# Performance work log

Hardware: AMD Instinct MI355X
Metric: run time of the kernel (lower is better)

Reference implementation:

```python
import math
import jax, jax.numpy as jnp
import numpy as np

N_HEADS = 32
N_KV_HEADS = 8
HEAD_DIM = 128
DIM = 4096
B = 32
MAX_SEQ = 4096
Q_LEN = 1
START_POS = 4095


def setup_inputs() -> dict:
    key = jax.random.key(0)
    ks = jax.random.split(key, 9)
    x = jax.random.normal(ks[0], (B, Q_LEN, DIM), dtype=jnp.float32)
    # RoPE angles for the current positions (seqlen=Q_LEN, half head_dim pairs)
    inv_freq = 1.0 / (500000.0 ** (np.arange(0, HEAD_DIM, 2, dtype=np.float32) / HEAD_DIM))
    pos = np.arange(START_POS, START_POS + Q_LEN, dtype=np.float32)
    ang = pos[:, None] * inv_freq[None, :]  # [Q_LEN, HEAD_DIM//2]
    freqs_cos = jnp.asarray(np.cos(ang), dtype=jnp.float32)
    freqs_sin = jnp.asarray(np.sin(ang), dtype=jnp.float32)
    cache_k = jax.random.normal(ks[1], (B, MAX_SEQ, N_KV_HEADS, HEAD_DIM), dtype=jnp.float32)
    cache_v = jax.random.normal(ks[2], (B, MAX_SEQ, N_KV_HEADS, HEAD_DIM), dtype=jnp.float32)
    s = 0.02
    wq = jax.random.normal(ks[3], (N_HEADS * HEAD_DIM, DIM), dtype=jnp.float32) * s
    wk = jax.random.normal(ks[4], (N_KV_HEADS * HEAD_DIM, DIM), dtype=jnp.float32) * s
    wv = jax.random.normal(ks[5], (N_KV_HEADS * HEAD_DIM, DIM), dtype=jnp.float32) * s
    wo = jax.random.normal(ks[6], (DIM, N_HEADS * HEAD_DIM), dtype=jnp.float32) * s
    return {"x": x, "start_pos": START_POS, "freqs_cos": freqs_cos, "freqs_sin": freqs_sin,
            "cache_k": cache_k, "cache_v": cache_v, "wq": wq, "wk": wk, "wv": wv, "wo": wo}


def _rope(t, cos, sin):
    # t: [B, S, h, hd]; cos/sin: [S, hd//2]; complex multiply on (even, odd) pairs
    tr = t.reshape(*t.shape[:-1], HEAD_DIM // 2, 2)
    a, b = tr[..., 0], tr[..., 1]
    c = cos[None, :, None, :]
    s = sin[None, :, None, :]
    out = jnp.stack([a * c - b * s, a * s + b * c], axis=-1)
    return out.reshape(t.shape)


def reference(x, start_pos, freqs_cos, freqs_sin, cache_k, cache_v, wq, wk, wv, wo):
    bsz, seqlen, _ = x.shape
    n_rep = N_HEADS // N_KV_HEADS
    xq = jnp.einsum('bsd,od->bso', x, wq).reshape(bsz, seqlen, N_HEADS, HEAD_DIM)
    xk = jnp.einsum('bsd,od->bso', x, wk).reshape(bsz, seqlen, N_KV_HEADS, HEAD_DIM)
    xv = jnp.einsum('bsd,od->bso', x, wv).reshape(bsz, seqlen, N_KV_HEADS, HEAD_DIM)
    xq = _rope(xq, freqs_cos, freqs_sin)
    xk = _rope(xk, freqs_cos, freqs_sin)
    # KV-cache update (start_pos is a static Python int)
    cache_k = cache_k.at[:, start_pos:start_pos + seqlen].set(xk)
    cache_v = cache_v.at[:, start_pos:start_pos + seqlen].set(xv)
    keys = cache_k[:, :start_pos + seqlen]    # [B, T, Hkv, hd]
    values = cache_v[:, :start_pos + seqlen]  # [B, T, Hkv, hd]
    # GQA: group query heads [H] -> [Hkv, n_rep]; avoids materializing repeated KV
    q = xq.reshape(bsz, seqlen, N_KV_HEADS, n_rep, HEAD_DIM)
    scale = 1.0 / math.sqrt(HEAD_DIM)
    scores = jnp.einsum('bsgrd,btgd->bgrst', q, keys) * scale  # [B, Hkv, n_rep, S, T]
    probs = jax.nn.softmax(scores, axis=-1)
    out = jnp.einsum('bgrst,btgd->bsgrd', probs, values)
    out = out.reshape(bsz, seqlen, N_HEADS * HEAD_DIM)
    return jnp.einsum('bse,de->bsd', out, wo)
```

## Files before the change

kernel.cpp:

```cpp
#include <hip/hip_runtime.h>

#define B_    32
#define DIM_  4096
#define NH_   32
#define NKV_  8
#define HD_   128
#define TSEQ  4096
#define NQKV  6144
#define GSPLIT 16
#define BK    32
#define NT    256
#define KRANGE (DIM_ / GSPLIT)
#define KTILES (KRANGE / BK)
#define TSPL  16
#define TS    256

typedef float f4_t __attribute__((ext_vector_type(4)));

__device__ __forceinline__ f4_t ntl(const float* p) {
    return __builtin_nontemporal_load((const f4_t*)p);
}

__global__ __launch_bounds__(256) void gemm32(
    const float* __restrict__ A, const float* __restrict__ w0,
    const float* __restrict__ w1, const float* __restrict__ w2,
    int b1, int b2, int N, float* __restrict__ po)
{
    __shared__ __align__(16) float wt[BK][NT + 4];
    __shared__ __align__(16) float xp[128][33];
    const int tid = threadIdx.x;
    const int cg  = tid & 63;
    const int bg  = tid >> 6;
    const int ct  = blockIdx.x * NT;
    const int k0  = blockIdx.y * KRANGE;

    const float* wb_; int c0_;
    if (ct < b1)      { wb_ = w0; c0_ = ct; }
    else if (ct < b2) { wb_ = w1; c0_ = ct - b1; }
    else              { wb_ = w2; c0_ = ct - b2; }

    const int kqx = (tid & 31) * 4;
    const int rrx = tid >> 5;
    const int kq2 = (tid & 7) * 4;
    const int rr2 = tid >> 3;

    f4_t xreg[4], wreg[8];

    #pragma unroll
    for (int st = 0; st < 4; ++st)
        xreg[st] = *(const f4_t*)(A + (size_t)(st * 8 + rrx) * DIM_ + k0 + kqx);
    #pragma unroll
    for (int st = 0; st < 8; ++st)
        wreg[st] = ntl(wb_ + (size_t)(c0_ + st * 32 + rr2) * DIM_ + k0 + kq2);
    #pragma unroll
    for (int st = 0; st < 4; ++st) {
        const int bb = st * 8 + rrx;
        xp[kqx + 0][bb] = xreg[st][0]; xp[kqx + 1][bb] = xreg[st][1];
        xp[kqx + 2][bb] = xreg[st][2]; xp[kqx + 3][bb] = xreg[st][3];
    }
    #pragma unroll
    for (int st = 0; st < 8; ++st) {
        const int c = st * 32 + rr2;
        wt[kq2 + 0][c] = wreg[st][0]; wt[kq2 + 1][c] = wreg[st][1];
        wt[kq2 + 2][c] = wreg[st][2]; wt[kq2 + 3][c] = wreg[st][3];
    }
    __syncthreads();

    float acc[8][4];
    #pragma unroll
    for (int i = 0; i < 8; ++i)
        #pragma unroll
        for (int j = 0; j < 4; ++j) acc[i][j] = 0.f;

    for (int tt = 0; tt < KTILES; ++tt) {
        if (tt < KTILES - 1) {
            #pragma unroll
            for (int st = 0; st < 8; ++st)
                wreg[st] = ntl(wb_ + (size_t)(c0_ + st * 32 + rr2) * DIM_
                               + k0 + (tt + 1) * BK + kq2);
        }
        if (tt == 3) {
            #pragma unroll
            for (int st = 0; st < 4; ++st)
                xreg[st] = *(const f4_t*)(A + (size_t)(st * 8 + rrx) * DIM_
                                          + k0 + 128 + kqx);
        }
        #pragma unroll 8
        for (int kk = 0; kk < BK; ++kk) {
            const int kr = (tt & 3) * BK + kk;
            const float4 xa = *(const float4*)&xp[kr][bg * 8];
            const float4 xb = *(const float4*)&xp[kr][bg * 8 + 4];
            const float4 wa = *(const float4*)&wt[kk][cg * 4];
            const float xv[8] = {xa.x, xa.y, xa.z, xa.w, xb.x, xb.y, xb.z, xb.w};
            const float wv[4] = {wa.x, wa.y, wa.z, wa.w};
            #pragma unroll
            for (int i = 0; i < 8; ++i)
                #pragma unroll
                for (int j = 0; j < 4; ++j)
                    acc[i][j] = fmaf(xv[i], wv[j], acc[i][j]);
        }
        __syncthreads();
        if (tt == 3) {
            #pragma unroll
            for (int st = 0; st < 4; ++st) {
                const int bb = st * 8 + rrx;
                xp[kqx + 0][bb] = xreg[st][0]; xp[kqx + 1][bb] = xreg[st][1];
                xp[kqx + 2][bb] = xreg[st][2]; xp[kqx + 3][bb] = xreg[st][3];
            }
        }
        if (tt < KTILES - 1) {
            #pragma unroll
            for (int st = 0; st < 8; ++st) {
                const int c = st * 32 + rr2;
                wt[kq2 + 0][c] = wreg[st][0]; wt[kq2 + 1][c] = wreg[st][1];
                wt[kq2 + 2][c] = wreg[st][2]; wt[kq2 + 3][c] = wreg[st][3];
            }
            __syncthreads();
        }
    }

    const size_t srow = (size_t)blockIdx.y * B_;
    #pragma unroll
    for (int i = 0; i < 8; ++i) {
        const int b = bg * 8 + i;
        const float4 o = make_float4(acc[i][0], acc[i][1], acc[i][2], acc[i][3]);
        *(float4*)&po[(srow + b) * N + ct + cg * 4] = o;
    }
}

__global__ void reduce_rope(const float* __restrict__ po,
                            const float* __restrict__ fc, const float* __restrict__ fs,
                            float* __restrict__ qkv)
{
    const int pid = blockIdx.x * 256 + threadIdx.x;
    const int b  = pid / (NQKV / 4);
    const int c0 = (pid - b * (NQKV / 4)) * 4;
    f4_t v = {0.f, 0.f, 0.f, 0.f};
    #pragma unroll
    for (int s = 0; s < GSPLIT; ++s)
        v += *(const f4_t*)(po + ((size_t)s * B_ + b) * NQKV + c0);
    if (c0 < DIM_ + NKV_ * HD_) {
        const int i = (c0 & 127) >> 1;
        const float ca = fc[i],     sa = fs[i];
        const float cb = fc[i + 1], sb = fs[i + 1];
        f4_t o;
        o[0] = v[0] * ca - v[1] * sa;
        o[1] = v[0] * sa + v[1] * ca;
        o[2] = v[2] * cb - v[3] * sb;
        o[3] = v[2] * sb + v[3] * cb;
        v = o;
    }
    *(f4_t*)(qkv + (size_t)b * NQKV + c0) = v;
}

__device__ __forceinline__ void attn_step(const f4_t kc, const f4_t vc,
                                          const f4_t* q, f4_t* acc, float* l)
{
    float p0 = kc[0]*q[0][0] + kc[1]*q[0][1] + kc[2]*q[0][2] + kc[3]*q[0][3];
    float p1 = kc[0]*q[1][0] + kc[1]*q[1][1] + kc[2]*q[1][2] + kc[3]*q[1][3];
    float p2 = kc[0]*q[2][0] + kc[1]*q[2][1] + kc[2]*q[2][2] + kc[3]*q[2][3];
    float p3 = kc[0]*q[3][0] + kc[1]*q[3][1] + kc[2]*q[3][2] + kc[3]*q[3][3];
    #pragma unroll
    for (int off = 1; off < 32; off <<= 1) {
        p0 += __shfl_xor(p0, off);
        p1 += __shfl_xor(p1, off);
        p2 += __shfl_xor(p2, off);
        p3 += __shfl_xor(p3, off);
    }
    const float scale = 0.08838834764831845f;
    p0 = __expf(p0 * scale); p1 = __expf(p1 * scale);
    p2 = __expf(p2 * scale); p3 = __expf(p3 * scale);
    l[0] += p0; l[1] += p1; l[2] += p2; l[3] += p3;
    acc[0] += p0 * vc; acc[1] += p1 * vc;
    acc[2] += p2 * vc; acc[3] += p3 * vc;
}

__global__ __launch_bounds__(256) void attn_partial(
    const float* __restrict__ qkv, const float* __restrict__ ck,
    const float* __restrict__ cv,
    float* __restrict__ po , float* __restrict__ pl )
{
    const int blk = blockIdx.x;
    const int s = blk & (TSPL - 1);
    const int b = blk / TSPL;
    const int tid  = threadIdx.x;
    const int g    = tid >> 5;
    const int lane = tid & 31;
    const int d4   = lane * 4;
    const float* qb = qkv + (size_t)b * NQKV;

    f4_t q[4];
    #pragma unroll
    for (int h = 0; h < 4; ++h)
        q[h] = *(const f4_t*)(qb + (g * 4 + h) * HD_ + d4);

    f4_t zero4 = {0.f, 0.f, 0.f, 0.f};
    f4_t acc[4] = {zero4, zero4, zero4, zero4};
    float l[4] = {0.f, 0.f, 0.f, 0.f};

    const int t0 = s * TS;
    const bool last = (s == TSPL - 1);
    const int niter = TS - (last ? 1 : 0);

    const size_t base = ((size_t)b * TSEQ + t0) * (NKV_ * HD_) + tid * 4;
    const float* kp = ck + base;
    const float* vp = cv + base;
    const int step = NKV_ * HD_;

    f4_t kc = ntl(kp), vc = ntl(vp);
    for (int it = 0; it < niter - 1; ++it) {
        kp += step; vp += step;
        const f4_t kn = ntl(kp);
        const f4_t vn = ntl(vp);
        attn_step(kc, vc, q, acc, l);
        kc = kn; vc = vn;
    }
    attn_step(kc, vc, q, acc, l);
    if (last) {
        const f4_t kf = *(const f4_t*)(qb + DIM_ + tid * 4);
        const f4_t vf = *(const f4_t*)(qb + DIM_ + NKV_ * HD_ + tid * 4);
        attn_step(kf, vf, q, acc, l);
    }

    float* pob = po + (((size_t)(b * NKV_ + g) * TSPL) + s) * 512;
    #pragma unroll
    for (int h = 0; h < 4; ++h)
        *(f4_t*)&pob[h * HD_ + d4] = acc[h];
    if (lane == 0) {
        float* plb = pl + ((size_t)(b * NKV_ + g) * TSPL + s) * 4;
        plb[0] = l[0]; plb[1] = l[1]; plb[2] = l[2]; plb[3] = l[3];
    }
}

__global__ void attn_combine(const float* __restrict__ po, const float* __restrict__ pl,
                             float* __restrict__ ao)
{
    const int bg  = blockIdx.x;
    const int tid = threadIdx.x;
    const int e0  = tid * 4;
    const int r   = e0 >> 7;
    f4_t o = {0.f, 0.f, 0.f, 0.f};
    float ls = 0.f;
    #pragma unroll 8
    for (int s = 0; s < TSPL; ++s) {
        o += *(const f4_t*)&po[((size_t)bg * TSPL + s) * 512 + e0];
        ls += pl[((size_t)bg * TSPL + s) * 4 + r];
    }
    o *= (1.f / ls);
    const int b = bg >> 3, g = bg & 7;
    *(f4_t*)&ao[(size_t)b * DIM_ + g * 512 + e0] = o;
}

__global__ void reduce_out(const float* __restrict__ po, float* __restrict__ out)
{
    const int pid = blockIdx.x * 256 + threadIdx.x;
    const int b  = pid >> 10;
    const int c0 = (pid & 1023) * 4;
    f4_t v = {0.f, 0.f, 0.f, 0.f};
    #pragma unroll
    for (int s = 0; s < GSPLIT; ++s)
        v += *(const f4_t*)(po + ((size_t)s * B_ + b) * DIM_ + c0);
    *(f4_t*)(out + (size_t)b * DIM_ + c0) = v;
}

extern "C" void kernel_launch(void* const* d_in, const int* in_sizes, int n_in,
                              void* d_out, int out_size, void* d_ws, size_t ws_size,
                              hipStream_t stream)
{
    (void)in_sizes; (void)n_in; (void)out_size; (void)ws_size;
    const float* x  = (const float*)d_in[0];
    const float* fc = (const float*)d_in[2];
    const float* fs = (const float*)d_in[3];
    const float* ck = (const float*)d_in[4];
    const float* cv = (const float*)d_in[5];
    const float* wq = (const float*)d_in[6];
    const float* wk = (const float*)d_in[7];
    const float* wv = (const float*)d_in[8];
    const float* wo = (const float*)d_in[9];
    float* out = (float*)d_out;
    float* ws  = (float*)d_ws;

    float* qkv  = ws;
    float* aout = ws + 196608;
    float* apo  = ws + 327680;
    float* apl  = ws + 2424832;
    float* gp   = ws + 2441216;

    gemm32<<<dim3(NQKV / NT, GSPLIT), 256, 0, stream>>>(
        x, wq, wk, wv, DIM_, DIM_ + NKV_ * HD_, NQKV, gp);
    reduce_rope<<<dim3(B_ * (NQKV / 4) / 256), 256, 0, stream>>>(gp, fc, fs, qkv);
    attn_partial<<<dim3(B_ * TSPL), 256, 0, stream>>>(qkv, ck, cv, apo, apl);
    attn_combine<<<dim3(B_ * NKV_), 128, 0, stream>>>(apo, apl, aout);
    gemm32<<<dim3(DIM_ / NT, GSPLIT), 256, 0, stream>>>(
        aout, wo, wo, wo, DIM_, DIM_, DIM_, gp);
    reduce_out<<<dim3(B_ * DIM_ / 4 / 256), 256, 0, stream>>>(gp, out);
}
```

Baseline: 274.2 us.

## Double split-K and sequence splits, shrink GEMM tiles, deepen KV prefetch

The GEMM now uses 128-column tiles with twice the K splits, so many more blocks are launched. Each block stages its whole K range of x into shared memory once instead of reloading it mid-loop. Attention splits the sequence into 32 chunks of 128 and prefetches K/V two steps ahead instead of one. The goal is better occupancy and latency hiding on a memory-bound decode step, at the cost of larger partial buffers and more reduction traffic in reduce_rope, attn_combine and reduce_out.

```diff
diff --git a/kernel.cpp b/kernel.cpp
--- a/kernel.cpp
+++ b/kernel.cpp
@@ -7,13 +7,13 @@
 #define HD_   128
 #define TSEQ  4096
 #define NQKV  6144
-#define GSPLIT 16
+#define GSPLIT 32
 #define BK    32
-#define NT    256
+#define NT    128
 #define KRANGE (DIM_ / GSPLIT)
 #define KTILES (KRANGE / BK)
-#define TSPL  16
-#define TS    256
+#define TSPL  32
+#define TS    128
 
 typedef float f4_t __attribute__((ext_vector_type(4)));
 
@@ -27,10 +27,10 @@
     int b1, int b2, int N, float* __restrict__ po)
 {
     __shared__ __align__(16) float wt[BK][NT + 4];
-    __shared__ __align__(16) float xp[128][33];
+    __shared__ __align__(16) float xp[KRANGE][33];
     const int tid = threadIdx.x;
-    const int cg  = tid & 63;
-    const int bg  = tid >> 6;
+    const int cg  = tid & 31;
+    const int bg  = tid >> 5;
     const int ct  = blockIdx.x * NT;
     const int k0  = blockIdx.y * KRANGE;
 
@@ -44,73 +44,56 @@
     const int kq2 = (tid & 7) * 4;
     const int rr2 = tid >> 3;
 
-    f4_t xreg[4], wreg[8];
-
-    #pragma unroll
-    for (int st = 0; st < 4; ++st)
-        xreg[st] = *(const f4_t*)(A + (size_t)(st * 8 + rrx) * DIM_ + k0 + kqx);
-    #pragma unroll
-    for (int st = 0; st < 8; ++st)
-        wreg[st] = ntl(wb_ + (size_t)(c0_ + st * 32 + rr2) * DIM_ + k0 + kq2);
+    f4_t wreg[4];
+
     #pragma unroll
     for (int st = 0; st < 4; ++st) {
         const int bb = st * 8 + rrx;
-        xp[kqx + 0][bb] = xreg[st][0]; xp[kqx + 1][bb] = xreg[st][1];
-        xp[kqx + 2][bb] = xreg[st][2]; xp[kqx + 3][bb] = xreg[st][3];
-    }
-    #pragma unroll
-    for (int st = 0; st < 8; ++st) {
+        const f4_t xv = *(const f4_t*)(A + (size_t)bb * DIM_ + k0 + kqx);
+        xp[kqx + 0][bb] = xv[0]; xp[kqx + 1][bb] = xv[1];
+        xp[kqx + 2][bb] = xv[2]; xp[kqx + 3][bb] = xv[3];
+    }
+    #pragma unroll
+    for (int st = 0; st < 4; ++st)
+        wreg[st] = ntl(wb_ + (size_t)(c0_ + st * 32 + rr2) * DIM_ + k0 + kq2);
+    #pragma unroll
+    for (int st = 0; st < 4; ++st) {
         const int c = st * 32 + rr2;
         wt[kq2 + 0][c] = wreg[st][0]; wt[kq2 + 1][c] = wreg[st][1];
         wt[kq2 + 2][c] = wreg[st][2]; wt[kq2 + 3][c] = wreg[st][3];
     }
     __syncthreads();
 
-    float acc[8][4];
-    #pragma unroll
-    for (int i = 0; i < 8; ++i)
+    float acc[4][4];
+    #pragma unroll
+    for (int i = 0; i < 4; ++i)
         #pragma unroll
         for (int j = 0; j < 4; ++j) acc[i][j] = 0.f;
 
     for (int tt = 0; tt < KTILES; ++tt) {
         if (tt < KTILES - 1) {
             #pragma unroll
-            for (int st = 0; st < 8; ++st)
+            for (int st = 0; st < 4; ++st)
                 wreg[st] = ntl(wb_ + (size_t)(c0_ + st * 32 + rr2) * DIM_
                                + k0 + (tt + 1) * BK + kq2);
         }
-        if (tt == 3) {
-            #pragma unroll
-            for (int st = 0; st < 4; ++st)
-                xreg[st] = *(const f4_t*)(A + (size_t)(st * 8 + rrx) * DIM_
-                                          + k0 + 128 + kqx);
-        }
         #pragma unroll 8
         for (int kk = 0; kk < BK; ++kk) {
-            const int kr = (tt & 3) * BK + kk;
-            const float4 xa = *(const float4*)&xp[kr][bg * 8];
-            const float4 xb = *(const float4*)&xp[kr][bg * 8 + 4];
+            const int kr = tt * BK + kk;
+            const float4 xa = *(const float4*)&xp[kr][bg * 4];
             const float4 wa = *(const float4*)&wt[kk][cg * 4];
-            const float xv[8] = {xa.x, xa.y, xa.z, xa.w, xb.x, xb.y, xb.z, xb.w};
+            const float xv[4] = {xa.x, xa.y, xa.z, xa.w};
             const float wv[4] = {wa.x, wa.y, wa.z, wa.w};
             #pragma unroll
-            for (int i = 0; i < 8; ++i)
+            for (int i = 0; i < 4; ++i)
                 #pragma unroll
                 for (int j = 0; j < 4; ++j)
                     acc[i][j] = fmaf(xv[i], wv[j], acc[i][j]);
         }
         __syncthreads();
-        if (tt == 3) {
+        if (tt < KTILES - 1) {
             #pragma unroll
             for (int st = 0; st < 4; ++st) {
-                const int bb = st * 8 + rrx;
-                xp[kqx + 0][bb] = xreg[st][0]; xp[kqx + 1][bb] = xreg[st][1];
-                xp[kqx + 2][bb] = xreg[st][2]; xp[kqx + 3][bb] = xreg[st][3];
-            }
-        }
-        if (tt < KTILES - 1) {
-            #pragma unroll
-            for (int st = 0; st < 8; ++st) {
                 const int c = st * 32 + rr2;
                 wt[kq2 + 0][c] = wreg[st][0]; wt[kq2 + 1][c] = wreg[st][1];
                 wt[kq2 + 2][c] = wreg[st][2]; wt[kq2 + 3][c] = wreg[st][3];
@@ -121,8 +104,8 @@
 
     const size_t srow = (size_t)blockIdx.y * B_;
     #pragma unroll
-    for (int i = 0; i < 8; ++i) {
-        const int b = bg * 8 + i;
+    for (int i = 0; i < 4; ++i) {
+        const int b = bg * 4 + i;
         const float4 o = make_float4(acc[i][0], acc[i][1], acc[i][2], acc[i][3]);
         *(float4*)&po[(srow + b) * N + ct + cg * 4] = o;
     }
@@ -208,14 +191,17 @@
     const int step = NKV_ * HD_;
 
     f4_t kc = ntl(kp), vc = ntl(vp);
-    for (int it = 0; it < niter - 1; ++it) {
+    kp += step; vp += step;
+    f4_t k1 = ntl(kp), v1 = ntl(vp);
+    for (int it = 0; it < niter - 2; ++it) {
         kp += step; vp += step;
-        const f4_t kn = ntl(kp);
-        const f4_t vn = ntl(vp);
+        const f4_t k2 = ntl(kp);
+        const f4_t v2 = ntl(vp);
         attn_step(kc, vc, q, acc, l);
-        kc = kn; vc = vn;
+        kc = k1; vc = v1; k1 = k2; v1 = v2;
     }
     attn_step(kc, vc, q, acc, l);
+    attn_step(k1, v1, q, acc, l);
     if (last) {
         const f4_t kf = *(const f4_t*)(qb + DIM_ + tid * 4);
         const f4_t vf = *(const f4_t*)(qb + DIM_ + NKV_ * HD_ + tid * 4);
@@ -283,8 +269,8 @@
     float* qkv  = ws;
     float* aout = ws + 196608;
     float* apo  = ws + 327680;
-    float* apl  = ws + 2424832;
-    float* gp   = ws + 2441216;
+    float* apl  = ws + 4521984;
+    float* gp   = ws + 4554752;
 
     gemm32<<<dim3(NQKV / NT, GSPLIT), 256, 0, stream>>>(
         x, wq, wk, wv, DIM_, DIM_ + NKV_ * HD_, NQKV, gp);
```

New measurement: 249.2 us. 1.1x faster.
